# Performance work log

Measured on AMD Instinct MI355X. Metric: run time of the kernel, lower is better.

The kernel has to match this reference:

```python
import jax, jax.numpy as jnp
import numpy as np

N_NODES = 100000
N_EDGES = 400000
HIDDEN = 256
N_LAYERS = 4
HEADS = 8
MAX_DEPTH = 20
NUM_GRAPHS = 128
SEQ_LEN = 5
VOCAB = 5002  # vocab_size + 2
NEG_SLOPE = 0.2
BN_EPS = 1e-5


def setup_inputs() -> dict:
    key = jax.random.key(0)
    ks = jax.random.split(key, 16)
    x = jax.random.randint(ks[0], (N_NODES, 2), 0, 98, dtype=jnp.int32)
    node_depth = jax.random.randint(ks[1], (N_NODES, 1), 0, MAX_DEPTH + 1, dtype=jnp.int32)
    edge_index = jax.random.randint(ks[2], (2, N_EDGES), 0, N_NODES, dtype=jnp.int32)
    batch = jnp.sort(jax.random.randint(ks[3], (N_NODES,), 0, NUM_GRAPHS, dtype=jnp.int32))
    s = 1.0 / np.sqrt(HIDDEN)
    return {
        "x": x,
        "node_depth": node_depth,
        "edge_index": edge_index,
        "batch": batch,
        "type_emb": jax.random.normal(ks[4], (98, HIDDEN), jnp.float32) * s,
        "attr_emb": jax.random.normal(ks[5], (10030, HIDDEN), jnp.float32) * s,
        "depth_emb": jax.random.normal(ks[6], (MAX_DEPTH + 1, HIDDEN), jnp.float32) * s,
        "Ws": jax.random.normal(ks[7], (N_LAYERS, HIDDEN, HIDDEN), jnp.float32) * s,
        "att_src": jax.random.normal(ks[8], (N_LAYERS, HIDDEN), jnp.float32) * s,
        "att_dst": jax.random.normal(ks[9], (N_LAYERS, HIDDEN), jnp.float32) * s,
        "gat_bias": jnp.zeros((N_LAYERS, HIDDEN), jnp.float32),
        "bn_gamma": jnp.ones((N_LAYERS, HIDDEN), jnp.float32),
        "bn_beta": jnp.zeros((N_LAYERS, HIDDEN), jnp.float32),
        "tok_W": jax.random.normal(ks[10], (SEQ_LEN, HIDDEN, VOCAB), jnp.float32) * s,
        "tok_b": jnp.zeros((SEQ_LEN, VOCAB), jnp.float32),
    }


def _gat_layer(h, src, dst, W, a_src, a_dst, bias, heads):
    # h: [N, HIDDEN]; PyG GATConv v1 with concat heads, self-loops already in (src, dst)
    N = h.shape[0]
    d = HIDDEN // heads
    hh = (h @ W).reshape(N, heads, d)                       # [N, H, d]
    s_src = jnp.einsum("nhd,hd->nh", hh, a_src.reshape(heads, d))
    s_dst = jnp.einsum("nhd,hd->nh", hh, a_dst.reshape(heads, d))
    e = jax.nn.leaky_relu(s_src[src] + s_dst[dst], NEG_SLOPE)  # [E, H]
    m = jax.ops.segment_max(e, dst, num_segments=N)           # [N, H]
    ex = jnp.exp(e - m[dst])
    denom = jax.ops.segment_sum(ex, dst, num_segments=N)      # [N, H]
    alpha = ex / denom[dst]                                    # [E, H]
    msg = hh[src] * alpha[:, :, None]                          # [E, H, d]
    out = jax.ops.segment_sum(msg, dst, num_segments=N)       # [N, H, d]
    return out.reshape(N, HIDDEN) + bias


def _batchnorm(h, gamma, beta):
    mu = jnp.mean(h, axis=0)
    var = jnp.var(h, axis=0)
    return (h - mu) * jax.lax.rsqrt(var + BN_EPS) * gamma + beta


def reference(x, node_depth, edge_index, batch, type_emb, attr_emb, depth_emb,
              Ws, att_src, att_dst, gat_bias, bn_gamma, bn_beta, tok_W, tok_b):
    N = x.shape[0]
    depth = jnp.minimum(node_depth.reshape(-1), MAX_DEPTH)
    h = type_emb[x[:, 0]] + attr_emb[x[:, 1]] + depth_emb[depth]  # [N, HIDDEN]

    # add self loops (PyG GATConv default)
    loop = jnp.arange(N, dtype=edge_index.dtype)
    src = jnp.concatenate([edge_index[0], loop])
    dst = jnp.concatenate([edge_index[1], loop])

    heads_per_layer = [HEADS] * (N_LAYERS - 1) + [1]
    for l in range(N_LAYERS):
        identity = h
        h = _gat_layer(h, src, dst, Ws[l], att_src[l], att_dst[l], gat_bias[l], heads_per_layer[l])
        h = _batchnorm(h, bn_gamma[l], bn_beta[l])
        h = jax.nn.relu(h)
        h = h + identity  # residual

    # mean pool per graph
    counts = jax.ops.segment_sum(jnp.ones((N,), h.dtype), batch, num_segments=NUM_GRAPHS)
    g = jax.ops.segment_sum(h, batch, num_segments=NUM_GRAPHS) / jnp.maximum(counts, 1.0)[:, None]

    # seq_len token predictors -> [SEQ_LEN, G, VOCAB]
    preds = jnp.einsum("gh,shv->sgv", g, tok_W) + tok_b[:, None, :]
    return preds
```

## Files before the change

### kernel.cpp

```cpp
#include <hip/hip_runtime.h>
#include <stdint.h>

typedef uint16_t u16;
typedef uint32_t u32;

#define N_NODESC 100000
#define N_EDGESC 400000
#define E_TOT    500000
#define HID      256
#define NLAYERS  4
#define NGRAPHS  128
#define SEQLEN   5
#define VOCABC   5002
#define MAXDEPTH 20
#define NEG_SLOPE 0.2f
#define BN_EPSC  1e-5f
#define NCHUNK   ((N_NODESC + 255)/256)
#define NCH64    ((N_NODESC + 63)/64)
#define NROWT    (N_NODESC/16)
#define NPART    64
#define NVQ      ((VOCABC + 63)/64)
#define ATTNB    2048
#define LDSROW   264

typedef __attribute__((ext_vector_type(8))) short short8;
typedef __attribute__((ext_vector_type(4))) float f32x4;
typedef __attribute__((ext_vector_type(4))) unsigned short u16x4;

__device__ __forceinline__ float b2f(u16 u){
  union { u32 i; float f; } v; v.i = ((u32)u) << 16; return v.f;
}
__device__ __forceinline__ u16 f2b(float f){
  union { float f; u32 i; } v; v.f = f;
  u32 u = v.i;
  u += 0x7FFFu + ((u >> 16) & 1u);
  return (u16)(u >> 16);
}
__device__ __forceinline__ float ldp(const void* p, size_t i, int f){
  return f ? ((const float*)p)[i] : b2f(((const u16*)p)[i]);
}
__device__ __forceinline__ f32x4 ld4(const void* p, size_t i, int f){
  f32x4 r;
  if (f){
    r = *(const f32x4*)((const float*)p + i);
  } else {
    const u16x4 u = *(const u16x4*)((const u16*)p + i);
    r[0] = b2f(u[0]); r[1] = b2f(u[1]); r[2] = b2f(u[2]); r[3] = b2f(u[3]);
  }
  return r;
}

__global__ __launch_bounds__(64) void k_detect(const void* temb, int* flag){
  int lane = threadIdx.x;
  const u32* w32 = (const u32*)temb;
  int sf = 0, sb = 0;
  for (int i = lane; i < 256; i += 64){
    u32 w = w32[i];
    union { u32 u; float f; } cf; cf.u = w;
    float af = fabsf(cf.f);
    if (cf.f == 0.0f || (af >= 1e-12f && af <= 4096.f)) sf++;
    float b0 = b2f((u16)(w & 0xFFFFu));
    float b1 = b2f((u16)(w >> 16));
    float a0 = fabsf(b0), a1 = fabsf(b1);
    if (b0 == 0.f || (a0 >= 1e-12f && a0 <= 4096.f)) sb++;
    if (b1 == 0.f || (a1 >= 1e-12f && a1 <= 4096.f)) sb++;
  }
  #pragma unroll
  for (int o = 1; o < 64; o <<= 1){ sf += __shfl_xor(sf, o); sb += __shfl_xor(sb, o); }
  if (lane == 0) *flag = (2*sf > sb) ? 1 : 0;
}

__global__ __launch_bounds__(256) void k_zero(int* __restrict__ p, int n){
  int i = blockIdx.x*256 + threadIdx.x;
  if (i < n) p[i] = 0;
}

__global__ __launch_bounds__(256) void k_embed(const int* __restrict__ x, const int* __restrict__ nd,
    const void* __restrict__ temb, const void* __restrict__ aemb, const void* __restrict__ demb,
    u16* __restrict__ h, const int* __restrict__ flagp, int* __restrict__ cursor){
  int f = *flagp;
  int tid = threadIdx.x;
  int r0 = blockIdx.x*64;
  if (tid < 64 && r0 + tid < N_NODESC) cursor[r0 + tid] = 0;
  int wid = tid >> 6, lane = tid & 63;
  int c4 = lane*4;
  #pragma unroll 4
  for (int k = 0; k < 16; ++k){
    int n = r0 + wid*16 + k;
    if (n >= N_NODESC) break;
    int t = x[n*2+0], a = x[n*2+1];
    if (t < 0) t = 0; if (t > 97) t = 97;
    if (a < 0) a = 0; if (a > 10029) a = 10029;
    int d = nd[n]; if (d > MAXDEPTH) d = MAXDEPTH; if (d < 0) d = 0;
    const f32x4 vt = ld4(temb, (size_t)t*HID + c4, f);
    const f32x4 va = ld4(aemb, (size_t)a*HID + c4, f);
    const f32x4 vd = ld4(demb, (size_t)d*HID + c4, f);
    u16x4 o;
    #pragma unroll
    for (int j = 0; j < 4; ++j) o[j] = f2b(vt[j] + va[j] + vd[j]);
    *(u16x4*)(h + (size_t)n*HID + c4) = o;
  }
}

__global__ __launch_bounds__(256) void k_hist(const int* __restrict__ ei, int* __restrict__ cnt){
  int e = blockIdx.x*256 + threadIdx.x;
  if (e >= E_TOT) return;
  int dst = (e < N_EDGESC) ? ei[N_EDGESC + e] : (e - N_EDGESC);
  if ((unsigned)dst >= N_NODESC) return;
  atomicAdd(&cnt[dst], 1);
}

__global__ __launch_bounds__(256) void k_scan_part(const int* __restrict__ cnt,
    int* __restrict__ off, int* __restrict__ btot){
  __shared__ int lds[256];
  int b = blockIdx.x, tid = threadIdx.x;
  int i = b*256 + tid;
  int v = (i < N_NODESC) ? cnt[i] : 0;
  lds[tid] = v;
  __syncthreads();
  #pragma unroll
  for (int s = 1; s < 256; s <<= 1){
    int t = (tid >= s) ? lds[tid - s] : 0;
    __syncthreads();
    lds[tid] += t;
    __syncthreads();
  }
  if (i < N_NODESC) off[i] = lds[tid] - v;
  if (tid == 255) btot[b] = lds[255];
}

__global__ __launch_bounds__(256) void k_scan_tot(const int* __restrict__ btot,
    int* __restrict__ boff, int* __restrict__ offN){
  __shared__ int lds[256];
  __shared__ int s_carry;
  int tid = threadIdx.x;
  if (tid == 0) s_carry = 0;
  __syncthreads();
  for (int base = 0; base < NCHUNK; base += 256){
    int i = base + tid;
    int v = (i < NCHUNK) ? btot[i] : 0;
    lds[tid] = v;
    __syncthreads();
    #pragma unroll
    for (int s = 1; s < 256; s <<= 1){
      int t = (tid >= s) ? lds[tid - s] : 0;
      __syncthreads();
      lds[tid] += t;
      __syncthreads();
    }
    if (i < NCHUNK) boff[i] = s_carry + lds[tid] - v;
    __syncthreads();
    if (tid == 255) s_carry += lds[255];
    __syncthreads();
  }
  if (tid == 0) *offN = s_carry;
}

__global__ __launch_bounds__(256) void k_scan_add(int* __restrict__ off,
    const int* __restrict__ boff, int* __restrict__ cursor){
  int b = blockIdx.x;
  int i = b*256 + threadIdx.x;
  if (i < N_NODESC){ off[i] += boff[b]; cursor[i] = 0; }
}

__global__ __launch_bounds__(256) void k_scatter(const int* __restrict__ ei,
    const int* __restrict__ soff, int* __restrict__ cursor, int* __restrict__ ssorted){
  int e = blockIdx.x*256 + threadIdx.x;
  if (e >= E_TOT) return;
  int src = (e < N_EDGESC) ? ei[e]            : (e - N_EDGESC);
  int dst = (e < N_EDGESC) ? ei[N_EDGESC + e] : (e - N_EDGESC);
  if ((unsigned)dst >= N_NODESC || (unsigned)src >= N_NODESC) return;
  int pos = soff[dst] + atomicAdd(&cursor[dst], 1);
  if ((unsigned)pos < E_TOT) ssorted[pos] = src;
}

__global__ __launch_bounds__(256) void k_transW(const void* __restrict__ W, u16* __restrict__ WT,
    const int* __restrict__ flagp){
  int f = *flagp;
  int l = blockIdx.y, n2 = blockIdx.x, k = threadIdx.x;
  WT[(l*HID + n2)*HID + k] = f2b(ldp(W, (size_t)(l*HID + k)*HID + n2, f));
}

__global__ __launch_bounds__(256) void k_prepVA(const void* __restrict__ Ws,
    const void* __restrict__ asrc, const void* __restrict__ adst,
    u16* __restrict__ VAT, const int* __restrict__ flagp){
  int f = *flagp;
  int l = blockIdx.x;
  int i = threadIdx.x;
  int H = (l == NLAYERS-1) ? 1 : 8;
  float col[16];
  #pragma unroll
  for (int c = 0; c < 16; ++c) col[c] = 0.f;
  if (H == 8){
    for (int h = 0; h < 8; ++h){
      float vs = 0.f, vd = 0.f;
      for (int o = h*32; o < h*32+32; ++o){
        float w = ldp(Ws, ((size_t)l*HID + i)*HID + o, f);
        vs += w * ldp(asrc, (size_t)l*HID + o, f);
        vd += w * ldp(adst, (size_t)l*HID + o, f);
      }
      col[h*2] = vs; col[h*2+1] = vd;
    }
  } else {
    float vs = 0.f, vd = 0.f;
    for (int o = 0; o < HID; ++o){
      float w = ldp(Ws, ((size_t)l*HID + i)*HID + o, f);
      vs += w * ldp(asrc, (size_t)l*HID + o, f);
      vd += w * ldp(adst, (size_t)l*HID + o, f);
    }
    col[0] = vs; col[1] = vd;
  }
  #pragma unroll
  for (int c = 0; c < 16; ++c)
    VAT[((size_t)l*16 + c)*HID + i] = f2b(col[c]);
}

__global__ __launch_bounds__(512) void k_gemm(u16* __restrict__ h,
    const u16* __restrict__ gout, const float* __restrict__ scale,
    const float* __restrict__ shift, int doApply,
    const u16* __restrict__ WT, const u16* __restrict__ VAT,
    u16* __restrict__ hh, float* __restrict__ ssrc, float* __restrict__ sdst,
    int H, float* __restrict__ bnpart){
  __shared__ u16 hA[2][16*LDSROW];
  int tid = threadIdx.x;
  if (blockIdx.x < NPART) bnpart[blockIdx.x*512 + tid] = 0.f;
  int wave = tid >> 6, lane = tid & 63;
  int m = lane & 15, quad = lane >> 4;
  int prow = tid >> 5, pch = (tid & 31)*8;

  short8 B[2][8];
  #pragma unroll
  for (int jj = 0; jj < 2; ++jj){
    const u16* wp = WT + (size_t)(((wave*2 + jj)*16 + m)*HID) + quad*8;
    #pragma unroll
    for (int ks = 0; ks < 8; ++ks)
      B[jj][ks] = *(const short8*)(wp + ks*32);
  }
  short8 B5[8];
  if (wave == 0){
    const u16* vp = VAT + (size_t)m*HID + quad*8;
    #pragma unroll
    for (int ks = 0; ks < 8; ++ks)
      B5[ks] = *(const short8*)(vp + ks*32);
  }

  f32x4 sc0 = {}, sc1 = {}, sh0 = {}, sh1 = {};
  if (doApply){
    sc0 = *(const f32x4*)(scale + pch);     sh0 = *(const f32x4*)(shift + pch);
    sc1 = *(const f32x4*)(scale + pch + 4); sh1 = *(const f32x4*)(shift + pch + 4);
  }

  int t = blockIdx.x;
  if (t >= NROWT) return;

  short8 h0, g0 = {};
  {
    size_t base = (size_t)(t*16 + prow)*HID + pch;
    h0 = *(const short8*)(h + base);
    if (doApply) g0 = *(const short8*)(gout + base);
  }

  int p = 0;
  for (;;){
    {
      size_t base = (size_t)(t*16 + prow)*HID + pch;
      if (doApply){
        #pragma unroll
        for (int j = 0; j < 4; ++j){
          float tv = b2f((u16)g0[j])*sc0[j] + sh0[j];
          tv = (tv > 0.f) ? tv : 0.f;
          h0[j] = (short)f2b(b2f((u16)h0[j]) + tv);
        }
        #pragma unroll
        for (int j = 0; j < 4; ++j){
          float tv = b2f((u16)g0[4+j])*sc1[j] + sh1[j];
          tv = (tv > 0.f) ? tv : 0.f;
          h0[4+j] = (short)f2b(b2f((u16)h0[4+j]) + tv);
        }
        *(short8*)(h + base) = h0;
      }
      *(short8*)(&hA[p][prow*LDSROW + pch]) = h0;
    }

    int tn = t + gridDim.x;
    bool hn = (tn < NROWT);
    short8 nh0 = h0, ng0 = g0;
    if (hn){
      size_t nbase = (size_t)(tn*16 + prow)*HID + pch;
      nh0 = *(const short8*)(h + nbase);
      if (doApply) ng0 = *(const short8*)(gout + nbase);
    }

    asm volatile("s_waitcnt lgkmcnt(0)" ::: "memory");
    __builtin_amdgcn_s_barrier();

    short8 A[8];
    #pragma unroll
    for (int ks = 0; ks < 8; ++ks)
      A[ks] = *(const short8*)(&hA[p][m*LDSROW + ks*32 + quad*8]);

    f32x4 acc0 = (f32x4){0.f,0.f,0.f,0.f};
    f32x4 acc1 = (f32x4){0.f,0.f,0.f,0.f};
    #pragma unroll
    for (int ks = 0; ks < 8; ++ks){
      acc0 = __builtin_amdgcn_mfma_f32_16x16x32_bf16(B[0][ks], A[ks], acc0, 0, 0, 0);
      acc1 = __builtin_amdgcn_mfma_f32_16x16x32_bf16(B[1][ks], A[ks], acc1, 0, 0, 0);
    }

    int node = t*16 + m;

    if (wave == 0){
      f32x4 acc5 = (f32x4){0.f,0.f,0.f,0.f};
      #pragma unroll
      for (int ks = 0; ks < 8; ++ks)
        acc5 = __builtin_amdgcn_mfma_f32_16x16x32_bf16(B5[ks], A[ks], acc5, 0, 0, 0);
      #pragma unroll
      for (int r = 0; r < 4; ++r){
        int c = quad*4 + r;
        float val = acc5[r];
        if (H == 8){
          int hidx = c >> 1;
          if ((c & 1) == 0) ssrc[node*8 + hidx] = val;
          else              sdst[node*8 + hidx] = val;
        } else {
          if (c == 0)      ssrc[node] = val;
          else if (c == 1) sdst[node] = val;
        }
      }
    }

    {
      int ch0 = (wave*2 + 0)*16 + quad*4;
      int ch1 = (wave*2 + 1)*16 + quad*4;
      u16x4 o0, o1;
      #pragma unroll
      for (int r = 0; r < 4; ++r){ o0[r] = f2b(acc0[r]); o1[r] = f2b(acc1[r]); }
      *(u16x4*)(hh + (size_t)node*HID + ch0) = o0;
      *(u16x4*)(hh + (size_t)node*HID + ch1) = o1;
    }

    if (!hn) break;
    t = tn; p ^= 1;
    h0 = nh0; g0 = ng0;
  }
}

__device__ __forceinline__ void attn_node(int n, int lane, const u16* __restrict__ hh,
    const float* __restrict__ ssrc, const float* __restrict__ sdst,
    const int* __restrict__ soff, const int* __restrict__ ssorted, int H, float r[4]){
  int f0 = lane*4;
  int hl = (H == 8) ? (lane >> 3) : 0;
  float sd = sdst[n*H + hl];
  int beg = soff[n], end = soff[n+1];
  if (beg < 0) beg = 0;
  if (end > E_TOT) end = E_TOT;
  r[0] = r[1] = r[2] = r[3] = 0.f;
  if (beg >= end) return;
  int src = ssorted[beg];
  if ((unsigned)src >= N_NODESC) src = n;
  u16x4 hvv = *(const u16x4*)(hh + (size_t)src*HID + f0);
  float es = ssrc[src*H + hl];
  float lval = 0.f;
  float o0 = 0.f, o1 = 0.f, o2 = 0.f, o3 = 0.f;
  for (int i = beg; i < end; ++i){
    int nsrc = src;
    if (i + 1 < end){
      nsrc = ssorted[i+1];
      if ((unsigned)nsrc >= N_NODESC) nsrc = src;
    }
    const u16x4 nh = *(const u16x4*)(hh + (size_t)nsrc*HID + f0);
    const float nes = ssrc[nsrc*H + hl];
    float ev = es + sd;
    ev = (ev > 0.f) ? ev : NEG_SLOPE*ev;
    ev = fminf(fmaxf(ev, -60.f), 60.f);
    float wv = __expf(ev);
    lval += wv;
    o0 += wv*b2f(hvv[0]);
    o1 += wv*b2f(hvv[1]);
    o2 += wv*b2f(hvv[2]);
    o3 += wv*b2f(hvv[3]);
    hvv = nh; es = nes;
  }
  float inv = (lval > 0.f) ? 1.f/lval : 0.f;
  r[0] = o0*inv; r[1] = o1*inv; r[2] = o2*inv; r[3] = o3*inv;
}

__global__ __launch_bounds__(256) void k_attn_gout(const u16* __restrict__ hh,
    const float* __restrict__ ssrc, const float* __restrict__ sdst,
    const int* __restrict__ soff, const int* __restrict__ ssorted,
    u16* __restrict__ gout, int H, float* __restrict__ bnpart){
  __shared__ float lsum[4*HID];
  __shared__ float lsq[4*HID];
  int wid = threadIdx.x >> 6, lane = threadIdx.x & 63;
  int f0 = lane*4;
  float s[4] = {0.f,0.f,0.f,0.f}, q[4] = {0.f,0.f,0.f,0.f};
  int gw = blockIdx.x*4 + wid;
  int nw = gridDim.x*4;
  for (int n = gw; n < N_NODESC; n += nw){
    float r[4];
    attn_node(n, lane, hh, ssrc, sdst, soff, ssorted, H, r);
    u16x4 o;
    #pragma unroll
    for (int j = 0; j < 4; ++j){
      o[j] = f2b(r[j]);
      s[j] += r[j];
      q[j] += r[j]*r[j];
    }
    *(u16x4*)(gout + (size_t)n*HID + f0) = o;
  }
  #pragma unroll
  for (int j = 0; j < 4; ++j){
    lsum[wid*HID + f0 + j] = s[j];
    lsq [wid*HID + f0 + j] = q[j];
  }
  __syncthreads();
  int c = threadIdx.x;
  float ts = lsum[c] + lsum[HID+c] + lsum[2*HID+c] + lsum[3*HID+c];
  float tq = lsq[c]  + lsq[HID+c]  + lsq[2*HID+c]  + lsq[3*HID+c];
  float* prow = bnpart + (size_t)(blockIdx.x & (NPART-1))*512;
  atomicAdd(&prow[c], ts);
  atomicAdd(&prow[HID + c], tq);
}

__global__ __launch_bounds__(256) void k_attn_stats(const u16* __restrict__ hh,
    const float* __restrict__ ssrc, const float* __restrict__ sdst,
    const int* __restrict__ soff, const int* __restrict__ ssorted,
    float* __restrict__ bnpart, int H){
  __shared__ float lsum[4*HID];
  __shared__ float lsq[4*HID];
  int wid = threadIdx.x >> 6, lane = threadIdx.x & 63;
  int gw = blockIdx.x*4 + wid;
  int nw = gridDim.x*4;
  float s[4] = {0.f,0.f,0.f,0.f}, q[4] = {0.f,0.f,0.f,0.f};
  for (int n = gw; n < N_NODESC; n += nw){
    float r[4];
    attn_node(n, lane, hh, ssrc, sdst, soff, ssorted, H, r);
    #pragma unroll
    for (int j = 0; j < 4; ++j){ s[j] += r[j]; q[j] += r[j]*r[j]; }
  }
  int f0 = lane*4;
  #pragma unroll
  for (int j = 0; j < 4; ++j){ lsum[wid*HID + f0 + j] = s[j]; lsq[wid*HID + f0 + j] = q[j]; }
  __syncthreads();
  int c = threadIdx.x;
  float ts = lsum[c] + lsum[HID+c] + lsum[2*HID+c] + lsum[3*HID+c];
  float tq = lsq[c]  + lsq[HID+c]  + lsq[2*HID+c]  + lsq[3*HID+c];
  float* prow = bnpart + (size_t)(blockIdx.x & (NPART-1))*512;
  atomicAdd(&prow[c], ts);
  atomicAdd(&prow[HID + c], tq);
}

__global__ __launch_bounds__(256) void k_attn_apply(const u16* __restrict__ hh,
    const float* __restrict__ ssrc, const float* __restrict__ sdst,
    const int* __restrict__ soff, const int* __restrict__ ssorted,
    const float* __restrict__ scale, const float* __restrict__ shift,
    u16* __restrict__ h, int H){
  int wid = threadIdx.x >> 6, lane = threadIdx.x & 63;
  int n = blockIdx.x*4 + wid;
  if (n >= N_NODESC) return;
  float r[4];
  attn_node(n, lane, hh, ssrc, sdst, soff, ssorted, H, r);
  int f0 = lane*4;
  const f32x4 sc = *(const f32x4*)(scale + f0);
  const f32x4 sh = *(const f32x4*)(shift + f0);
  u16x4 hv = *(u16x4*)(h + (size_t)n*HID + f0);
  u16x4 o;
  #pragma unroll
  for (int j = 0; j < 4; ++j){
    float t = r[j]*sc[j] + sh[j];
    t = (t > 0.f) ? t : 0.f;
    o[j] = f2b(b2f(hv[j]) + t);
  }
  *(u16x4*)(h + (size_t)n*HID + f0) = o;
}

__global__ __launch_bounds__(256) void k_bn_final(const float* __restrict__ bnpart,
    const void* __restrict__ gamma, const void* __restrict__ beta,
    float* __restrict__ scale, float* __restrict__ shift,
    const int* __restrict__ flagp, int loff){
  int f = *flagp;
  int c = threadIdx.x;
  float s = 0.f, q = 0.f;
  #pragma unroll 4
  for (int p = 0; p < NPART; ++p){
    s += bnpart[(size_t)p*512 + c];
    q += bnpart[(size_t)p*512 + HID + c];
  }
  float mu  = s * (1.f/N_NODESC);
  float var = q * (1.f/N_NODESC) - mu*mu;
  if (!(var >= 0.f)) var = 0.f;
  float sc = ldp(gamma, (size_t)loff + c, f) * rsqrtf(var + BN_EPSC);
  scale[c] = sc;
  shift[c] = ldp(beta, (size_t)loff + c, f) - mu*sc;
}

__global__ __launch_bounds__(256) void k_pool(const u16* __restrict__ h,
    const int* __restrict__ batch, float* __restrict__ gsum, int* __restrict__ gcnt){
  int c = threadIdx.x;
  int r0 = blockIdx.x * 256;
  int r1 = min(r0 + 256, N_NODESC);
  if (r0 >= N_NODESC) return;
  int cur = batch[r0];
  float acc = 0.f;
  int nacc = 0;
  for (int r = r0; r < r1; ++r){
    int b = batch[r];
    if ((unsigned)b >= NGRAPHS) continue;
    if (b != cur){
      if ((unsigned)cur < NGRAPHS){
        atomicAdd(&gsum[cur*HID + c], acc);
        if (c == 0) atomicAdd(&gcnt[cur], nacc);
      }
      acc = 0.f; nacc = 0; cur = b;
    }
    acc += b2f(h[(size_t)r*HID + c]);
    nacc++;
  }
  if ((unsigned)cur < NGRAPHS){
    atomicAdd(&gsum[cur*HID + c], acc);
    if (c == 0) atomicAdd(&gcnt[cur], nacc);
  }
}

__global__ __launch_bounds__(256) void k_pool_fused(const u16* __restrict__ h,
    const u16* __restrict__ gout, const float* __restrict__ scale, const float* __restrict__ shift,
    const int* __restrict__ batch, float* __restrict__ gsum, int* __restrict__ gcnt){
  __shared__ int lb[64];
  int tid = threadIdx.x;
  int r0 = blockIdx.x*64;
  if (tid < 64){
    int rr = r0 + tid;
    lb[tid] = (rr < N_NODESC) ? batch[rr] : -1;
  }
  __syncthreads();
  int wid = tid >> 6, lane = tid & 63;
  int c4 = lane*4;
  const f32x4 sc = *(const f32x4*)(scale + c4);
  const f32x4 sh = *(const f32x4*)(shift + c4);
  int rbase = r0 + wid*16;
  f32x4 acc = (f32x4){0.f,0.f,0.f,0.f};
  int nacc = 0, cur = -1;
  #pragma unroll 4
  for (int k = 0; k < 16; ++k){
    int r = rbase + k;
    if (r >= N_NODESC) break;
    int b = lb[wid*16 + k];
    if ((unsigned)b >= NGRAPHS) continue;
    if (b != cur){
      if ((unsigned)cur < NGRAPHS){
        atomicAdd(&gsum[cur*HID + c4+0], acc[0]);
        atomicAdd(&gsum[cur*HID + c4+1], acc[1]);
        atomicAdd(&gsum[cur*HID + c4+2], acc[2]);
        atomicAdd(&gsum[cur*HID + c4+3], acc[3]);
        if (lane == 0) atomicAdd(&gcnt[cur], nacc);
      }
      acc = (f32x4){0.f,0.f,0.f,0.f}; nacc = 0; cur = b;
    }
    const u16x4 hv = *(const u16x4*)(h    + (size_t)r*HID + c4);
    const u16x4 gv = *(const u16x4*)(gout + (size_t)r*HID + c4);
    #pragma unroll
    for (int j = 0; j < 4; ++j){
      float t = b2f(gv[j])*sc[j] + sh[j];
      t = (t > 0.f) ? t : 0.f;
      acc[j] += b2f(hv[j]) + t;
    }
    nacc++;
  }
  if ((unsigned)cur < NGRAPHS){
    atomicAdd(&gsum[cur*HID + c4+0], acc[0]);
    atomicAdd(&gsum[cur*HID + c4+1], acc[1]);
    atomicAdd(&gsum[cur*HID + c4+2], acc[2]);
    atomicAdd(&gsum[cur*HID + c4+3], acc[3]);
    if (lane == 0) atomicAdd(&gcnt[cur], nacc);
  }
}

__global__ __launch_bounds__(256) void k_gprep(const float* __restrict__ gsum,
    const int* __restrict__ gcnt, u16* __restrict__ gbf){
  int g = blockIdx.x, c = threadIdx.x;
  int cc = gcnt[g]; if (cc < 1) cc = 1;
  gbf[g*HID + c] = f2b(gsum[(size_t)g*HID + c] * (1.f/(float)cc));
}

__global__ __launch_bounds__(256) void k_pred(const u16* __restrict__ gbf,
    const void* __restrict__ tokW, const void* __restrict__ tokb, void* __restrict__ out,
    const int* __restrict__ flagp){
  int f = *flagp;
  int wave = threadIdx.x >> 6, lane = threadIdx.x & 63;
  int m = lane & 15, quad = lane >> 4;
  int s = blockIdx.y;
  int v = blockIdx.x*64 + wave*16 + m;
  bool vok = (v < VOCABC);

  f32x4 acc[8];
  #pragma unroll
  for (int t = 0; t < 8; ++t) acc[t] = (f32x4){0.f,0.f,0.f,0.f};

  const size_t wrow = (size_t)s*HID*VOCABC + v;
  #pragma unroll
  for (int ks = 0; ks < 8; ++ks){
    int kb = ks*32 + quad*8;
    short8 b;
    #pragma unroll
    for (int j = 0; j < 8; ++j)
      b[j] = vok ? (short)f2b(ldp(tokW, wrow + (size_t)(kb + j)*VOCABC, f)) : (short)0;
    #pragma unroll
    for (int t = 0; t < 8; ++t){
      const short8 a = *(const short8*)(gbf + (size_t)(t*16 + m)*HID + kb);
      acc[t] = __builtin_amdgcn_mfma_f32_16x16x32_bf16(a, b, acc[t], 0, 0, 0);
    }
  }

  float bb = vok ? ldp(tokb, (size_t)s*VOCABC + v, f) : 0.f;
  if (!vok) return;
  #pragma unroll
  for (int t = 0; t < 8; ++t){
    #pragma unroll
    for (int r = 0; r < 4; ++r){
      int grow = t*16 + quad*4 + r;
      float val = acc[t][r] + bb;
      size_t oi = ((size_t)(s*NGRAPHS + grow)*VOCABC) + v;
      if (f) ((float*)out)[oi] = val;
      else   ((u16*)out)[oi]   = f2b(val);
    }
  }
}

extern "C" void kernel_launch(void* const* d_in, const int* in_sizes, int n_in,
                              void* d_out, int out_size, void* d_ws, size_t ws_size,
                              hipStream_t stream) {
  const int* x          = (const int*)d_in[0];
  const int* node_depth = (const int*)d_in[1];
  const int* edge_index = (const int*)d_in[2];
  const int* batch      = (const int*)d_in[3];
  const void* type_emb  = d_in[4];
  const void* attr_emb  = d_in[5];
  const void* depth_emb = d_in[6];
  const void* Ws        = d_in[7];
  const void* att_src   = d_in[8];
  const void* att_dst   = d_in[9];
  const void* bn_gamma  = d_in[11];
  const void* bn_beta   = d_in[12];
  const void* tok_W     = d_in[13];
  const void* tok_b     = d_in[14];

  char* base = (char*)d_ws;
  size_t off = 0;
  auto carve = [&](size_t bytes) -> void* {
    void* p = base + off;
    off += (bytes + 255) & ~(size_t)255;
    return p;
  };
  u16*   h     = (u16*)carve((size_t)N_NODESC*HID*2);
  u16*   hh    = (u16*)carve((size_t)N_NODESC*HID*2);
  float* ssrc  = (float*)carve((size_t)N_NODESC*8*4);
  float* sdst  = (float*)carve((size_t)N_NODESC*8*4);
  int*   soff  = (int*)carve((size_t)(N_NODESC+1)*4);
  int*   cursor= (int*)carve((size_t)N_NODESC*4);
  int*   ssorted=(int*)carve((size_t)E_TOT*4);
  int*   btot  = (int*)carve((size_t)NCHUNK*4);
  int*   boff  = (int*)carve((size_t)NCHUNK*4);
  u16*   WT    = (u16*)carve((size_t)NLAYERS*HID*HID*2);
  u16*   VAT   = (u16*)carve((size_t)NLAYERS*16*HID*2);
  float* bnpart= (float*)carve((size_t)NPART*512*4);
  float* bnscale=(float*)carve(HID*4);
  float* bnshift=(float*)carve(HID*4);
  float* gsum  = (float*)carve((size_t)NGRAPHS*HID*4);
  int*   gcnt  = (int*)carve((size_t)NGRAPHS*4);
  u16*   gbf   = (u16*)carve((size_t)NGRAPHS*HID*2);
  int*   dflag = (int*)carve(256);
  size_t common = off;
  u16*   gout  = (u16*)carve((size_t)N_NODESC*HID*2);
  const bool useGout = (off <= ws_size);
  if (common > ws_size) return;

  const int EB  = (E_TOT + 255)/256;
  const int NB4 = (N_NODESC + 3)/4;

  k_detect<<<1, 64, 0, stream>>>(type_emb, dflag);

  k_embed<<<NCH64, 256, 0, stream>>>(x, node_depth, type_emb, attr_emb, depth_emb, h, dflag, cursor);
  k_transW<<<dim3(256, NLAYERS), 256, 0, stream>>>(Ws, WT, dflag);
  k_prepVA<<<NLAYERS, 256, 0, stream>>>(Ws, att_src, att_dst, VAT, dflag);
  k_hist<<<EB, 256, 0, stream>>>(edge_index, cursor);
  k_scan_part<<<NCHUNK, 256, 0, stream>>>(cursor, soff, btot);
  k_scan_tot<<<1, 256, 0, stream>>>(btot, boff, soff + N_NODESC);
  k_scan_add<<<NCHUNK, 256, 0, stream>>>(soff, boff, cursor);
  k_scatter<<<EB, 256, 0, stream>>>(edge_index, soff, cursor, ssorted);

  for (int l = 0; l < NLAYERS; ++l){
    int H = (l == NLAYERS-1) ? 1 : 8;
    int doApply = (useGout && l > 0) ? 1 : 0;
    k_gemm<<<1024, 512, 0, stream>>>(h, gout, bnscale, bnshift, doApply,
                                     WT + (size_t)l*HID*HID, VAT + (size_t)l*16*HID,
                                     hh, ssrc, sdst, H, bnpart);
    if (useGout){
      k_attn_gout<<<ATTNB, 256, 0, stream>>>(hh, ssrc, sdst, soff, ssorted, gout, H, bnpart);
      k_bn_final<<<1, 256, 0, stream>>>(bnpart, bn_gamma, bn_beta, bnscale, bnshift, dflag, l*HID);
    } else {
      k_attn_stats<<<2048, 256, 0, stream>>>(hh, ssrc, sdst, soff, ssorted, bnpart, H);
      k_bn_final<<<1, 256, 0, stream>>>(bnpart, bn_gamma, bn_beta, bnscale, bnshift, dflag, l*HID);
      k_attn_apply<<<NB4, 256, 0, stream>>>(hh, ssrc, sdst, soff, ssorted, bnscale, bnshift, h, H);
    }
  }

  k_zero<<<(NGRAPHS*HID + NGRAPHS + 255)/256, 256, 0, stream>>>((int*)gsum, NGRAPHS*HID + NGRAPHS);
  if (useGout)
    k_pool_fused<<<NCH64, 256, 0, stream>>>(h, gout, bnscale, bnshift, batch, gsum, gcnt);
  else
    k_pool<<<NCHUNK, 256, 0, stream>>>(h, batch, gsum, gcnt);
  k_gprep<<<NGRAPHS, 256, 0, stream>>>(gsum, gcnt, gbf);

  k_pred<<<dim3(NVQ, SEQLEN), 256, 0, stream>>>(gbf, tok_W, tok_b, d_out, dflag);
}
```

Before: 783.9 us.

## Batch four edge gathers per iteration in GAT attention with deeper prefetch

Restructures the per-node attention aggregation to load four neighbor rows and scores at once, prefetching indices two batches ahead and the next node's CSR offsets one node ahead. The goal is more memory-level parallelism to hide the latency of the dependent gather chain. It also pre-scales the attention scores by log2(e) so a raw v_exp_f32 can replace __expf, and templates on the head count. In exchange it uses more registers and does masked work on tail edges, and the exp clamp changes slightly.

```diff
diff --git a/kernel.cpp b/kernel.cpp
--- a/kernel.cpp
+++ b/kernel.cpp
@@ -15,6 +15,7 @@
 #define MAXDEPTH 20
 #define NEG_SLOPE 0.2f
 #define BN_EPSC  1e-5f
+#define LOG2E    1.4426950408889634f
 #define NCHUNK   ((N_NODESC + 255)/256)
 #define NCH64    ((N_NODESC + 63)/64)
 #define NROWT    (N_NODESC/16)
@@ -35,6 +36,11 @@
   u32 u = v.i;
   u += 0x7FFFu + ((u >> 16) & 1u);
   return (u16)(u >> 16);
+}
+__device__ __forceinline__ float fexp2(float x){
+  float r;
+  asm("v_exp_f32 %0, %1\n\ts_nop 0" : "=v"(r) : "v"(x));
+  return r;
 }
 __device__ __forceinline__ float ldp(const void* p, size_t i, int f){
   return f ? ((const float*)p)[i] : b2f(((const u16*)p)[i]);
@@ -317,7 +323,7 @@
       #pragma unroll
       for (int r = 0; r < 4; ++r){
         int c = quad*4 + r;
-        float val = acc5[r];
+        float val = acc5[r] * LOG2E;
         if (H == 8){
           int hidx = c >> 1;
           if ((c & 1) == 0) ssrc[node*8 + hidx] = val;
@@ -345,44 +351,121 @@
   }
 }
 
-__device__ __forceinline__ void attn_node(int n, int lane, const u16* __restrict__ hh,
-    const float* __restrict__ ssrc, const float* __restrict__ sdst,
-    const int* __restrict__ soff, const int* __restrict__ ssorted, int H, float r[4]){
-  int f0 = lane*4;
-  int hl = (H == 8) ? (lane >> 3) : 0;
+__device__ __forceinline__ void attn_acc(u16x4 v, float es, float sd, bool valid,
+    float& lval, float& o0, float& o1, float& o2, float& o3){
+  float ev = es + sd;
+  ev = fmaxf(ev, NEG_SLOPE*ev);
+  ev = fminf(fmaxf(ev, -87.f), 87.f);
+  float wv = fexp2(ev);
+  wv = valid ? wv : 0.f;
+  lval += wv;
+  o0 += wv*b2f(v[0]);
+  o1 += wv*b2f(v[1]);
+  o2 += wv*b2f(v[2]);
+  o3 += wv*b2f(v[3]);
+}
+
+template<int H>
+__device__ __forceinline__ void attn_node(int n, int lane, int beg, int end,
+    const u16* __restrict__ hh, const float* __restrict__ ssrc,
+    const float* __restrict__ sdst, const int* __restrict__ ssorted, float r[4]){
+  const int f0 = lane*4;
+  const int hl = (H == 8) ? (lane >> 3) : 0;
   float sd = sdst[n*H + hl];
-  int beg = soff[n], end = soff[n+1];
   if (beg < 0) beg = 0;
   if (end > E_TOT) end = E_TOT;
   r[0] = r[1] = r[2] = r[3] = 0.f;
   if (beg >= end) return;
-  int src = ssorted[beg];
-  if ((unsigned)src >= N_NODESC) src = n;
-  u16x4 hvv = *(const u16x4*)(hh + (size_t)src*HID + f0);
-  float es = ssrc[src*H + hl];
-  float lval = 0.f;
-  float o0 = 0.f, o1 = 0.f, o2 = 0.f, o3 = 0.f;
-  for (int i = beg; i < end; ++i){
-    int nsrc = src;
-    if (i + 1 < end){
-      nsrc = ssorted[i+1];
-      if ((unsigned)nsrc >= N_NODESC) nsrc = src;
-    }
-    const u16x4 nh = *(const u16x4*)(hh + (size_t)nsrc*HID + f0);
-    const float nes = ssrc[nsrc*H + hl];
-    float ev = es + sd;
-    ev = (ev > 0.f) ? ev : NEG_SLOPE*ev;
-    ev = fminf(fmaxf(ev, -60.f), 60.f);
-    float wv = __expf(ev);
-    lval += wv;
-    o0 += wv*b2f(hvv[0]);
-    o1 += wv*b2f(hvv[1]);
-    o2 += wv*b2f(hvv[2]);
-    o3 += wv*b2f(hvv[3]);
-    hvv = nh; es = nes;
+  const int last = end - 1;
+
+  int a0 = ssorted[beg];
+  int a1 = ssorted[min(beg+1,last)];
+  int a2 = ssorted[min(beg+2,last)];
+  int a3 = ssorted[min(beg+3,last)];
+  a0 = ((unsigned)a0 < N_NODESC) ? a0 : n;
+  a1 = ((unsigned)a1 < N_NODESC) ? a1 : n;
+  a2 = ((unsigned)a2 < N_NODESC) ? a2 : n;
+  a3 = ((unsigned)a3 < N_NODESC) ? a3 : n;
+  u16x4 v0 = *(const u16x4*)(hh + (size_t)a0*HID + f0);
+  u16x4 v1 = *(const u16x4*)(hh + (size_t)a1*HID + f0);
+  u16x4 v2 = *(const u16x4*)(hh + (size_t)a2*HID + f0);
+  u16x4 v3 = *(const u16x4*)(hh + (size_t)a3*HID + f0);
+  float e0 = ssrc[a0*H + hl];
+  float e1 = ssrc[a1*H + hl];
+  float e2 = ssrc[a2*H + hl];
+  float e3 = ssrc[a3*H + hl];
+  int b0 = 0, b1 = 0, b2 = 0, b3 = 0;
+  if (end - beg > 4){
+    b0 = ssorted[min(beg+4,last)];
+    b1 = ssorted[min(beg+5,last)];
+    b2 = ssorted[min(beg+6,last)];
+    b3 = ssorted[min(beg+7,last)];
+  }
+
+  float lval = 0.f, o0 = 0.f, o1 = 0.f, o2 = 0.f, o3 = 0.f;
+  for (int i = beg; ; i += 4){
+    bool more = (i + 4 < end);
+    u16x4 w0, w1, w2, w3;
+    float x0, x1, x2, x3;
+    int c0, c1, c2, c3;
+    if (more){
+      c0 = ssorted[min(i+8,last)];
+      c1 = ssorted[min(i+9,last)];
+      c2 = ssorted[min(i+10,last)];
+      c3 = ssorted[min(i+11,last)];
+      int g0 = ((unsigned)b0 < N_NODESC) ? b0 : n;
+      int g1 = ((unsigned)b1 < N_NODESC) ? b1 : n;
+      int g2 = ((unsigned)b2 < N_NODESC) ? b2 : n;
+      int g3 = ((unsigned)b3 < N_NODESC) ? b3 : n;
+      w0 = *(const u16x4*)(hh + (size_t)g0*HID + f0);
+      w1 = *(const u16x4*)(hh + (size_t)g1*HID + f0);
+      w2 = *(const u16x4*)(hh + (size_t)g2*HID + f0);
+      w3 = *(const u16x4*)(hh + (size_t)g3*HID + f0);
+      x0 = ssrc[g0*H + hl];
+      x1 = ssrc[g1*H + hl];
+      x2 = ssrc[g2*H + hl];
+      x3 = ssrc[g3*H + hl];
+    }
+    attn_acc(v0, e0, sd, true,        lval, o0, o1, o2, o3);
+    attn_acc(v1, e1, sd, (i+1) < end, lval, o0, o1, o2, o3);
+    attn_acc(v2, e2, sd, (i+2) < end, lval, o0, o1, o2, o3);
+    attn_acc(v3, e3, sd, (i+3) < end, lval, o0, o1, o2, o3);
+    if (!more) break;
+    v0 = w0; v1 = w1; v2 = w2; v3 = w3;
+    e0 = x0; e1 = x1; e2 = x2; e3 = x3;
+    b0 = c0; b1 = c1; b2 = c2; b3 = c3;
   }
   float inv = (lval > 0.f) ? 1.f/lval : 0.f;
   r[0] = o0*inv; r[1] = o1*inv; r[2] = o2*inv; r[3] = o3*inv;
+}
+
+template<int H>
+__device__ __forceinline__ void attn_gout_loop(const u16* __restrict__ hh,
+    const float* __restrict__ ssrc, const float* __restrict__ sdst,
+    const int* __restrict__ soff, const int* __restrict__ ssorted,
+    u16* __restrict__ gout, float s[4], float q[4]){
+  int wid = threadIdx.x >> 6, lane = threadIdx.x & 63;
+  int f0 = lane*4;
+  int gw = blockIdx.x*4 + wid;
+  int nw = gridDim.x*4;
+  int beg = 0, end = 0;
+  if (gw < N_NODESC){ beg = soff[gw]; end = soff[gw+1]; }
+  for (int n = gw; n < N_NODESC; n += nw){
+    int n2 = n + nw;
+    int pb = 0, pe = 0;
+    if (n2 < N_NODESC){ pb = soff[n2]; pe = soff[n2+1]; }
+    float r[4];
+    attn_node<H>(n, lane, beg, end, hh, ssrc, sdst, ssorted, r);
+    u16x4 o;
+    #pragma unroll
+    for (int j = 0; j < 4; ++j){
+      o[j] = f2b(r[j]);
+      s[j] += r[j];
+      q[j] += r[j]*r[j];
+    }
+    *(u16x4*)(gout + (size_t)n*HID + f0) = o;
+    beg = pb; end = pe;
+  }
 }
 
 __global__ __launch_bounds__(256) void k_attn_gout(const u16* __restrict__ hh,
@@ -394,20 +477,8 @@
   int wid = threadIdx.x >> 6, lane = threadIdx.x & 63;
   int f0 = lane*4;
   float s[4] = {0.f,0.f,0.f,0.f}, q[4] = {0.f,0.f,0.f,0.f};
-  int gw = blockIdx.x*4 + wid;
-  int nw = gridDim.x*4;
-  for (int n = gw; n < N_NODESC; n += nw){
-    float r[4];
-    attn_node(n, lane, hh, ssrc, sdst, soff, ssorted, H, r);
-    u16x4 o;
-    #pragma unroll
-    for (int j = 0; j < 4; ++j){
-      o[j] = f2b(r[j]);
-      s[j] += r[j];
-      q[j] += r[j]*r[j];
-    }
-    *(u16x4*)(gout + (size_t)n*HID + f0) = o;
-  }
+  if (H == 8) attn_gout_loop<8>(hh, ssrc, sdst, soff, ssorted, gout, s, q);
+  else        attn_gout_loop<1>(hh, ssrc, sdst, soff, ssorted, gout, s, q);
   #pragma unroll
   for (int j = 0; j < 4; ++j){
     lsum[wid*HID + f0 + j] = s[j];
@@ -422,6 +493,28 @@
   atomicAdd(&prow[HID + c], tq);
 }
 
+template<int H>
+__device__ __forceinline__ void attn_stats_loop(const u16* __restrict__ hh,
+    const float* __restrict__ ssrc, const float* __restrict__ sdst,
+    const int* __restrict__ soff, const int* __restrict__ ssorted,
+    float s[4], float q[4]){
+  int wid = threadIdx.x >> 6, lane = threadIdx.x & 63;
+  int gw = blockIdx.x*4 + wid;
+  int nw = gridDim.x*4;
+  int beg = 0, end = 0;
+  if (gw < N_NODESC){ beg = soff[gw]; end = soff[gw+1]; }
+  for (int n = gw; n < N_NODESC; n += nw){
+    int n2 = n + nw;
+    int pb = 0, pe = 0;
+    if (n2 < N_NODESC){ pb = soff[n2]; pe = soff[n2+1]; }
+    float r[4];
+    attn_node<H>(n, lane, beg, end, hh, ssrc, sdst, ssorted, r);
+    #pragma unroll
+    for (int j = 0; j < 4; ++j){ s[j] += r[j]; q[j] += r[j]*r[j]; }
+    beg = pb; end = pe;
+  }
+}
+
 __global__ __launch_bounds__(256) void k_attn_stats(const u16* __restrict__ hh,
     const float* __restrict__ ssrc, const float* __restrict__ sdst,
     const int* __restrict__ soff, const int* __restrict__ ssorted,
@@ -429,15 +522,9 @@
   __shared__ float lsum[4*HID];
   __shared__ float lsq[4*HID];
   int wid = threadIdx.x >> 6, lane = threadIdx.x & 63;
-  int gw = blockIdx.x*4 + wid;
-  int nw = gridDim.x*4;
   float s[4] = {0.f,0.f,0.f,0.f}, q[4] = {0.f,0.f,0.f,0.f};
-  for (int n = gw; n < N_NODESC; n += nw){
-    float r[4];
-    attn_node(n, lane, hh, ssrc, sdst, soff, ssorted, H, r);
-    #pragma unroll
-    for (int j = 0; j < 4; ++j){ s[j] += r[j]; q[j] += r[j]*r[j]; }
-  }
+  if (H == 8) attn_stats_loop<8>(hh, ssrc, sdst, soff, ssorted, s, q);
+  else        attn_stats_loop<1>(hh, ssrc, sdst, soff, ssorted, s, q);
   int f0 = lane*4;
   #pragma unroll
   for (int j = 0; j < 4; ++j){ lsum[wid*HID + f0 + j] = s[j]; lsq[wid*HID + f0 + j] = q[j]; }
@@ -458,8 +545,10 @@
   int wid = threadIdx.x >> 6, lane = threadIdx.x & 63;
   int n = blockIdx.x*4 + wid;
   if (n >= N_NODESC) return;
+  int beg = soff[n], end = soff[n+1];
   float r[4];
-  attn_node(n, lane, hh, ssrc, sdst, soff, ssorted, H, r);
+  if (H == 8) attn_node<8>(n, lane, beg, end, hh, ssrc, sdst, ssorted, r);
+  else        attn_node<1>(n, lane, beg, end, hh, ssrc, sdst, ssorted, r);
   int f0 = lane*4;
   const f32x4 sc = *(const f32x4*)(scale + f0);
   const f32x4 sh = *(const f32x4*)(shift + f0);
```

After: 813.0 us. 1.04x slower.
